# Optimization experiments

Measured on AMD Instinct MI355X. Metric: run time of the kernel, lower is better.

The kernel has to match this reference:

```python
import jax, jax.numpy as jnp
import numpy as np
import math

DEPTH = 3
NUM_GRAPHS = 8
BN_EPS = 1e-5
POOL_RATIO = 0.5


def _gcn(A, x, W, b):
    # GCNConv(improved=True): A_hat = A + 2*I; out = D^-1/2 A_hat D^-1/2 (x W) + b
    n = A.shape[0]
    A_hat = A + 2.0 * jnp.eye(n, dtype=A.dtype)
    deg = A_hat.sum(axis=1)
    d = jnp.where(deg > 0, jax.lax.rsqrt(deg), 0.0)
    return d[:, None] * (A_hat @ (d[:, None] * (x @ W))) + b


def _bn_eval(x, g, b):
    # BatchNorm1d in eval mode with running_mean=0, running_var=1
    return x * (g / jnp.sqrt(1.0 + BN_EPS)) + b


def _forward(x, edge_index, batch, conv0_w, conv0_b, down_w, down_b, pool_w,
             up_w, up_b, lins_w, lins_b, bn_g, bn_b, out_w, out_b):
    n0 = x.shape[0]
    # dense weighted adjacency A[dst, src] += 1 (duplicates sum, same as scatter-add MP)
    A = jnp.zeros((n0, n0), x.dtype).at[edge_index[1], edge_index[0]].add(1.0)

    # ---- GraphUNet (eval mode: dropout p=0.92 is identity) ----
    h = jax.nn.relu(_gcn(A, x, conv0_w, conv0_b))
    xs, As, perms = [h], [A], []
    for i in range(DEPTH):
        n = A.shape[0]
        eye = jnp.eye(n, dtype=A.dtype)
        S = A + eye                       # add_self_loops(weight=1)
        A2 = (S @ S) * (1.0 - eye)        # spspmm then remove_self_loops
        # TopKPooling: score = tanh((x.w)/||w||), keep top ceil(0.5*n) nodes
        score = jnp.tanh((h @ pool_w[i]) / jnp.linalg.norm(pool_w[i]))
        k = math.ceil(POOL_RATIO * n)
        _, perm = jax.lax.top_k(score, k)
        h = h[perm] * score[perm][:, None]
        A = A2[perm][:, perm]             # filter_adj
        h = jax.nn.relu(_gcn(A, h, down_w[i], down_b[i]))
        if i < DEPTH - 1:
            xs.append(h)
            As.append(A)
        perms.append(perm)
    for i in range(DEPTH):
        j = DEPTH - 1 - i
        res, Aj, perm = xs[j], As[j], perms[j]
        up = jnp.zeros_like(res).at[perm].set(h)
        h = res + up                      # sum_res=True skip connection
        h = _gcn(Aj, h, up_w[i], up_b[i])
        if i < DEPTH - 1:
            h = jax.nn.relu(h)

    # ---- global_add_pool + BN/Linear/tanh head ----
    g = jax.ops.segment_sum(h, batch, num_segments=NUM_GRAPHS)
    for i in range(3):
        g = _bn_eval(g, bn_g[i], bn_b[i])
        g = jnp.tanh(g @ lins_w[i] + lins_b[i])
    g = _bn_eval(g, bn_g[3], bn_b[3])
    return g @ out_w + out_b


def setup_inputs() -> dict:
    key = jax.random.key(0)
    ks = jax.random.split(key, 20)
    N, F, H, O, E = 4096, 64, 128, 32, 65536
    s = 0.05
    x = jax.random.normal(ks[0], (N, F), jnp.float32)
    src = jax.random.randint(ks[1], (E,), 0, N)
    dst = jax.random.randint(ks[2], (E,), 0, N)
    edge_index = jnp.stack([jnp.concatenate([src, dst]),
                            jnp.concatenate([dst, src])]).astype(jnp.int32)
    batch = jnp.sort(jax.random.randint(ks[3], (N,), 0, NUM_GRAPHS)).astype(jnp.int32)
    return {
        "x": x,
        "edge_index": edge_index,
        "batch": batch,
        "conv0_w": jax.random.normal(ks[4], (F, H), jnp.float32) * s,
        "conv0_b": jnp.zeros((H,), jnp.float32),
        "down_w": jax.random.normal(ks[5], (DEPTH, H, H), jnp.float32) * s,
        "down_b": jnp.zeros((DEPTH, H), jnp.float32),
        "pool_w": jax.random.normal(ks[6], (DEPTH, H), jnp.float32),
        "up_w": jax.random.normal(ks[7], (DEPTH, H, H), jnp.float32) * s,
        "up_b": jnp.zeros((DEPTH, H), jnp.float32),
        "lins_w": jax.random.normal(ks[8], (3, H, H), jnp.float32) * s,
        "lins_b": jnp.zeros((3, H), jnp.float32),
        "bn_g": jnp.ones((4, H), jnp.float32),
        "bn_b": jnp.zeros((4, H), jnp.float32),
        "out_w": jax.random.normal(ks[9], (H, O), jnp.float32) * s,
        "out_b": jnp.zeros((O,), jnp.float32),
    }


def reference(x, edge_index, batch, conv0_w, conv0_b, down_w, down_b, pool_w,
              up_w, up_b, lins_w, lins_b, bn_g, bn_b, out_w, out_b):
    return _forward(x, edge_index, batch, conv0_w, conv0_b, down_w, down_b,
                    pool_w, up_w, up_b, lins_w, lins_b, bn_g, bn_b, out_w, out_b)
```

## Files before the change

kernel.cpp:

```cpp
#include <hip/hip_runtime.h>
#include <math.h>

#define H 128
#define NG 8

typedef __attribute__((ext_vector_type(8))) short bf16x8;
typedef __attribute__((ext_vector_type(8))) unsigned short ushort8;
typedef __attribute__((ext_vector_type(4))) float f32x4;

static __device__ __forceinline__ float b2f(unsigned short u) {
  union { unsigned int i; float f; } v;
  v.i = ((unsigned int)u) << 16;
  return v.f;
}
static __device__ __forceinline__ unsigned short f2b(float f) {
  return (unsigned short)(__float_as_uint(f) >> 16);
}

__global__ void k_hist(const int* __restrict__ ei, int E, int* __restrict__ cnt) {
  int e = blockIdx.x * 256 + threadIdx.x;
  if (e >= E) return;
  atomicAdd(&cnt[ei[E + e]], 1);
}

__global__ __launch_bounds__(1024) void k_scan(const int* __restrict__ cnt,
                                               int* __restrict__ rowptr,
                                               float* __restrict__ dv, int n) {
  __shared__ int sums[1024];
  int tid = threadIdx.x;
  int base = tid * 4;
  int v0 = 0, v1 = 0, v2 = 0, v3 = 0;
  if (base < n) { v0 = cnt[base]; v1 = cnt[base + 1]; v2 = cnt[base + 2]; v3 = cnt[base + 3]; }
  int s = v0 + v1 + v2 + v3;
  sums[tid] = s;
  __syncthreads();
  for (int off = 1; off < 1024; off <<= 1) {
    int t = (tid >= off) ? sums[tid - off] : 0;
    __syncthreads();
    sums[tid] += t;
    __syncthreads();
  }
  int excl = sums[tid] - s;
  if (base < n) {
    rowptr[base] = excl;
    rowptr[base + 1] = excl + v0;
    rowptr[base + 2] = excl + v0 + v1;
    rowptr[base + 3] = excl + v0 + v1 + v2;
    dv[base] = rsqrtf((float)v0 + 2.0f);
    dv[base + 1] = rsqrtf((float)v1 + 2.0f);
    dv[base + 2] = rsqrtf((float)v2 + 2.0f);
    dv[base + 3] = rsqrtf((float)v3 + 2.0f);
  }
  if (tid == 1023) rowptr[n] = sums[1023];
}

__global__ void k_fill(const int* __restrict__ ei, int E, const int* __restrict__ rowptr,
                       int* __restrict__ cursor, int* __restrict__ colidx) {
  int e = blockIdx.x * 256 + threadIdx.x;
  if (e >= E) return;
  int r = ei[E + e], c = ei[e];
  int p = atomicAdd(&cursor[r], 1);
  colidx[rowptr[r] + p] = c;
}

template <int MODE, int RS, int EMIT>
__global__ __launch_bounds__(256) void k_xw(const float* __restrict__ X,
                                            const float* __restrict__ W,
                                            const float* __restrict__ dv,
                                            const int* __restrict__ idx,
                                            const float* __restrict__ aux,
                                            float* __restrict__ Y,
                                            unsigned short* __restrict__ YT,
                                            int n, int F) {
  __shared__ float Xs[64][36];
  __shared__ float Ws[32][132];
  __shared__ int ridx[64];
  __shared__ float rscl[64];
  int tid = threadIdx.x;
  int rowBase = blockIdx.x * 64;
  if (MODE == 1) {
    if (tid < 64) {
      int pp = idx[rowBase + tid];
      ridx[tid] = pp;
      rscl[tid] = aux[pp];
    }
  } else if (MODE == 2) {
    if (tid < 64) ridx[tid] = idx[rowBase + tid];
  }
  if (MODE != 0) __syncthreads();
  int r0 = (tid >> 5) << 3;
  int c0 = (tid & 31) << 2;
  float acc[8][4] = {};
  for (int k0 = 0; k0 < F; k0 += 32) {
#pragma unroll
    for (int it = 0, e = tid; it < 8; ++it, e += 256) {
      int ii = e >> 5, kk = e & 31;
      int gk = k0 + kk;
      float v;
      if (MODE == 0) {
        v = X[(size_t)(rowBase + ii) * F + gk];
      } else if (MODE == 1) {
        v = X[(size_t)ridx[ii] * F + gk] * rscl[ii];
      } else {
        v = X[(size_t)(rowBase + ii) * F + gk];
        int iv = ridx[ii];
        if (iv >= 0) v += aux[(size_t)iv * H + gk];
      }
      Xs[ii][kk] = v;
    }
#pragma unroll
    for (int it = 0, e = tid; it < 4; ++it, e += 256) {
      int kk = e >> 5, cc4 = e & 31;
      *(float4*)&Ws[kk][cc4 << 2] = *(const float4*)&W[(size_t)(k0 + kk) * H + (cc4 << 2)];
    }
    __syncthreads();
#pragma unroll
    for (int kk = 0; kk < 32; kk += 4) {
      float4 a4[8], w4[4];
#pragma unroll
      for (int i = 0; i < 8; ++i) a4[i] = *(const float4*)&Xs[r0 + i][kk];
#pragma unroll
      for (int s = 0; s < 4; ++s) w4[s] = *(const float4*)&Ws[kk + s][c0];
#pragma unroll
      for (int i = 0; i < 8; ++i) {
        float av[4] = {a4[i].x, a4[i].y, a4[i].z, a4[i].w};
#pragma unroll
        for (int s = 0; s < 4; ++s) {
          float wv[4] = {w4[s].x, w4[s].y, w4[s].z, w4[s].w};
#pragma unroll
          for (int j = 0; j < 4; ++j) acc[i][j] = fmaf(av[s], wv[j], acc[i][j]);
        }
      }
    }
    __syncthreads();
  }
  float vout[8][4];
#pragma unroll
  for (int i = 0; i < 8; ++i) {
    int row = rowBase + r0 + i;
    float d = RS ? rsqrtf(dv[row] + 2.0f) : dv[row];
#pragma unroll
    for (int j = 0; j < 4; ++j) vout[i][j] = d * acc[i][j];
    *(float4*)&Y[(size_t)row * H + c0] =
        make_float4(vout[i][0], vout[i][1], vout[i][2], vout[i][3]);
  }
  if (EMIT) {
#pragma unroll
    for (int j = 0; j < 4; ++j) {
      ushort8 hi, lo;
#pragma unroll
      for (int i = 0; i < 8; ++i) {
        float v = vout[i][j];
        unsigned short hh = f2b(v);
        hi[i] = hh;
        lo[i] = f2b(v - b2f(hh));
      }
      int c = c0 + j;
      *(ushort8*)&YT[(size_t)c * (2 * n) + rowBase + r0] = hi;
      *(ushort8*)&YT[(size_t)c * (2 * n) + n + rowBase + r0] = lo;
    }
  }
}

template <int SCORE>
__global__ void k_spmm_fin(const int* __restrict__ rowptr, const int* __restrict__ colidx,
                           const float* __restrict__ Y, const float* __restrict__ dv,
                           const float* __restrict__ bias, float* __restrict__ Out,
                           const float* __restrict__ w, float* __restrict__ score,
                           int n, int relu) {
  __shared__ float wn;
  int tid = threadIdx.x;
  if (SCORE) {
    if (tid < 64) {
      float s = w[tid] * w[tid] + w[tid + 64] * w[tid + 64];
#pragma unroll
      for (int o = 32; o > 0; o >>= 1) s += __shfl_down(s, o);
      if (tid == 0) wn = sqrtf(s);
    }
    __syncthreads();
  }
  int row = blockIdx.x * 4 + (tid >> 6);
  int lane = tid & 63;
  if (row >= n) return;
  int s = rowptr[row], e = rowptr[row + 1];
  int c2 = lane * 2;
  float a0 = 0.f, a1 = 0.f;
  int i = s;
  for (; i + 1 < e; i += 2) {
    int cA = colidx[i], cB = colidx[i + 1];
    float2 yA = *(const float2*)&Y[(size_t)cA * H + c2];
    float2 yB = *(const float2*)&Y[(size_t)cB * H + c2];
    a0 += yA.x + yB.x;
    a1 += yA.y + yB.y;
  }
  if (i < e) {
    int c = colidx[i];
    float2 y = *(const float2*)&Y[(size_t)c * H + c2];
    a0 += y.x;
    a1 += y.y;
  }
  float d = dv[row];
  float2 yr = *(const float2*)&Y[(size_t)row * H + c2];
  float v0 = d * (a0 + 2.0f * yr.x) + bias[c2];
  float v1 = d * (a1 + 2.0f * yr.y) + bias[c2 + 1];
  if (relu) { v0 = fmaxf(v0, 0.f); v1 = fmaxf(v1, 0.f); }
  *(float2*)&Out[(size_t)row * H + c2] = make_float2(v0, v1);
  if (SCORE) {
    float sc = v0 * w[c2] + v1 * w[c2 + 1];
#pragma unroll
    for (int o = 32; o > 0; o >>= 1) sc += __shfl_down(sc, o);
    if (lane == 0) score[row] = tanhf(sc / wn);
  }
}

__global__ __launch_bounds__(256) void k_ata_rows(const int* __restrict__ rowptr,
                                                  const int* __restrict__ colidx,
                                                  const int* __restrict__ perm,
                                                  const int* __restrict__ inv,
                                                  unsigned short* __restrict__ Ab,
                                                  float* __restrict__ dv, int kdim) {
  __shared__ int acc[2048];
  __shared__ int wsum[4];
  int i = blockIdx.x;
  int tid = threadIdx.x;
  for (int j = tid; j < kdim; j += 256) acc[j] = 0;
  __syncthreads();
  int p = perm[i];
  int s = rowptr[p], e = rowptr[p + 1];
  int deg = e - s;
  int wave = tid >> 6, lane = tid & 63;
  for (int q = wave; q <= deg; q += 4) {
    int kn = (q < deg) ? colidx[s + q] : p;
    int s2 = rowptr[kn], e2 = rowptr[kn + 1];
    for (int idx = s2 + lane; idx <= e2; idx += 64) {
      int j = (idx < e2) ? colidx[idx] : kn;
      int ii = inv[j];
      if (ii >= 0) atomicAdd(&acc[ii], 1);
    }
  }
  __syncthreads();
  int rs = 0;
  {
    int j0 = tid * 8;
    ushort8 v;
#pragma unroll
    for (int q = 0; q < 8; ++q) {
      int j = j0 + q;
      int c = (j == i) ? 0 : acc[j];
      rs += c;
      v[q] = f2b((float)c);
    }
    *(ushort8*)&Ab[(size_t)i * kdim + j0] = v;
  }
#pragma unroll
  for (int o = 32; o > 0; o >>= 1) rs += __shfl_down(rs, o);
  if (lane == 0) wsum[wave] = rs;
  __syncthreads();
  if (tid == 0) dv[i] = rsqrtf((float)(wsum[0] + wsum[1] + wsum[2] + wsum[3]) + 2.0f);
}

__global__ __launch_bounds__(256) void k_ata_mfma_g(const unsigned short* __restrict__ Ab,
                                                    const int* __restrict__ perm,
                                                    float* __restrict__ PartC,
                                                    int n, int k, int KC) {
  __shared__ __align__(16) unsigned short As[64][64];
  __shared__ __align__(16) unsigned short Bs[64][64];
  __shared__ int pr[64], pc[64];
  int tid = threadIdx.x;
  int w = tid >> 6, ln = tid & 63;
  int l15 = ln & 15, l4 = ln >> 4;
  int br = blockIdx.y, bc = blockIdx.x;
  if (tid < 64) pr[tid] = perm[br * 64 + tid];
  else if (tid < 128) pc[tid - 64] = perm[bc * 64 + (tid - 64)];
  __syncthreads();
  f32x4 acc[4] = {};
  int k0s = blockIdx.z * KC;
  for (int k0 = k0s; k0 < k0s + KC; k0 += 64) {
#pragma unroll
    for (int it = 0; it < 2; ++it) {
      int e = tid + it * 256;
      int row = e >> 3, ch = e & 7;
      int sch = (ch ^ (row & 7)) * 8;
      int base = k0 + ch * 8;
      {
        int p = pr[row];
        ushort8 v = *(const ushort8*)&Ab[(size_t)p * n + base];
#pragma unroll
        for (int q = 0; q < 8; ++q)
          if (base + q == p) v[q] = f2b(b2f(v[q]) + 1.0f);
        *(ushort8*)&As[row][sch] = v;
      }
      {
        int p = pc[row];
        ushort8 v = *(const ushort8*)&Ab[(size_t)p * n + base];
#pragma unroll
        for (int q = 0; q < 8; ++q)
          if (base + q == p) v[q] = f2b(b2f(v[q]) + 1.0f);
        *(ushort8*)&Bs[row][sch] = v;
      }
    }
    __syncthreads();
#pragma unroll
    for (int s = 0; s < 2; ++s) {
      int arow = w * 16 + l15;
      bf16x8 af = *(const bf16x8*)&As[arow][((s * 4 + l4) ^ (arow & 7)) * 8];
#pragma unroll
      for (int f = 0; f < 4; ++f) {
        int brow = f * 16 + l15;
        bf16x8 bfr = *(const bf16x8*)&Bs[brow][((s * 4 + l4) ^ (brow & 7)) * 8];
        acc[f] = __builtin_amdgcn_mfma_f32_16x16x32_bf16(af, bfr, acc[f], 0, 0, 0);
      }
    }
    __syncthreads();
  }
  float* out = PartC + (size_t)blockIdx.z * k * k;
#pragma unroll
  for (int f = 0; f < 4; ++f) {
#pragma unroll
    for (int r = 0; r < 4; ++r) {
      int gi = br * 64 + w * 16 + l4 * 4 + r;
      int gj = bc * 64 + f * 16 + l15;
      out[(size_t)gi * k + gj] = acc[f][r];
    }
  }
}

__global__ __launch_bounds__(256) void k_ata_sk_part(const float* __restrict__ A,
                                                     const int* __restrict__ perm,
                                                     float* __restrict__ PartC,
                                                     int n, int k, int CK) {
  int bc = blockIdx.x, br = blockIdx.y;
  __shared__ float As[64][36];
  __shared__ float Bs[64][36];
  __shared__ int pr[64], pc[64];
  int tid = threadIdx.x;
  if (tid < 64) pr[tid] = perm[br * 64 + tid];
  else if (tid < 128) pc[tid - 64] = perm[bc * 64 + (tid - 64)];
  __syncthreads();
  int ty = tid >> 4;
  int tx = tid & 15;
  float acc[4][4] = {};
  int k0s = blockIdx.z * CK;
  for (int k0 = k0s; k0 < k0s + CK; k0 += 32) {
#pragma unroll
    for (int it = 0, e = tid; it < 8; ++it, e += 256) {
      int ii = e >> 5, kk = e & 31;
      int gk = k0 + kk;
      int p = pr[ii];
      As[ii][kk] = A[(size_t)p * n + gk] + ((p == gk) ? 1.0f : 0.0f);
      p = pc[ii];
      Bs[ii][kk] = A[(size_t)p * n + gk] + ((p == gk) ? 1.0f : 0.0f);
    }
    __syncthreads();
#pragma unroll
    for (int kk = 0; kk < 32; kk += 4) {
      float4 a4[4], b4[4];
#pragma unroll
      for (int i = 0; i < 4; ++i) a4[i] = *(const float4*)&As[ty + 16 * i][kk];
#pragma unroll
      for (int j = 0; j < 4; ++j) b4[j] = *(const float4*)&Bs[tx + 16 * j][kk];
#pragma unroll
      for (int i = 0; i < 4; ++i) {
        float av[4] = {a4[i].x, a4[i].y, a4[i].z, a4[i].w};
#pragma unroll
        for (int j = 0; j < 4; ++j) {
          float bv[4] = {b4[j].x, b4[j].y, b4[j].z, b4[j].w};
#pragma unroll
          for (int s = 0; s < 4; ++s) acc[i][j] = fmaf(av[s], bv[s], acc[i][j]);
        }
      }
    }
    __syncthreads();
  }
  float* out = PartC + (size_t)blockIdx.z * k * k;
#pragma unroll
  for (int i = 0; i < 4; ++i) {
    int gi = br * 64 + ty + 16 * i;
#pragma unroll
    for (int j = 0; j < 4; ++j) {
      int gj = bc * 64 + tx + 16 * j;
      out[(size_t)gi * k + gj] = acc[i][j];
    }
  }
}

template <int NCH>
__global__ void k_ata_fin(const float* __restrict__ PartC, float* __restrict__ C,
                          float* __restrict__ rowsum, int k) {
  __shared__ float wsum[4];
  int gi = blockIdx.x;
  int tid = threadIdx.x;
  int j4 = tid * 4;
  size_t stride = (size_t)k * k;
  size_t off = (size_t)gi * k + j4;
  float4 s = *(const float4*)&PartC[off];
#pragma unroll
  for (int z = 1; z < NCH; ++z) {
    float4 p = *(const float4*)&PartC[z * stride + off];
    s.x += p.x; s.y += p.y; s.z += p.z; s.w += p.w;
  }
  if (gi >= j4 && gi < j4 + 4) ((float*)&s)[gi - j4] = 0.0f;
  *(float4*)&C[off] = s;
  float part = s.x + s.y + s.z + s.w;
  int lane = tid & 63, wave = tid >> 6;
#pragma unroll
  for (int o = 32; o > 0; o >>= 1) part += __shfl_down(part, o);
  if (lane == 0) wsum[wave] = part;
  __syncthreads();
  if (tid == 0) {
    int nw = blockDim.x >> 6;
    float t = 0.f;
    for (int q = 0; q < nw; ++q) t += wsum[q];
    rowsum[gi] = t;
  }
}

__global__ __launch_bounds__(256) void k_gcn_mfma(const unsigned short* __restrict__ A,
                                                  const unsigned short* __restrict__ YT,
                                                  float* __restrict__ Part, int n, int VK) {
  __shared__ __align__(16) unsigned short As[64][64];
  __shared__ __align__(16) unsigned short Bs[128][64];
  int tid = threadIdx.x;
  int w = tid >> 6, ln = tid & 63;
  int l15 = ln & 15, l4 = ln >> 4;
  int rowBase = blockIdx.x * 64;
  float* out = Part + (size_t)blockIdx.y * n * H;
  f32x4 acc[8] = {};
  int vk0s = blockIdx.y * VK;
  for (int vk0 = vk0s; vk0 < vk0s + VK; vk0 += 64) {
    int ka = vk0 & (n - 1);
#pragma unroll
    for (int it = 0; it < 2; ++it) {
      int e = tid + it * 256;
      int row = e >> 3, ch = e & 7;
      int sch = (ch ^ (row & 7)) * 8;
      *(ushort8*)&As[row][sch] = *(const ushort8*)&A[(size_t)(rowBase + row) * n + ka + ch * 8];
    }
#pragma unroll
    for (int it = 0; it < 4; ++it) {
      int e = tid + it * 256;
      int row = e >> 3, ch = e & 7;
      int sch = (ch ^ (row & 7)) * 8;
      *(ushort8*)&Bs[row][sch] = *(const ushort8*)&YT[(size_t)row * (2 * n) + vk0 + ch * 8];
    }
    __syncthreads();
#pragma unroll
    for (int s = 0; s < 2; ++s) {
      int arow = w * 16 + l15;
      bf16x8 af = *(const bf16x8*)&As[arow][((s * 4 + l4) ^ (arow & 7)) * 8];
#pragma unroll
      for (int f = 0; f < 8; ++f) {
        int brow = f * 16 + l15;
        bf16x8 bfr = *(const bf16x8*)&Bs[brow][((s * 4 + l4) ^ (brow & 7)) * 8];
        acc[f] = __builtin_amdgcn_mfma_f32_16x16x32_bf16(af, bfr, acc[f], 0, 0, 0);
      }
    }
    __syncthreads();
  }
#pragma unroll
  for (int f = 0; f < 8; ++f) {
#pragma unroll
    for (int r = 0; r < 4; ++r) {
      int row = rowBase + w * 16 + l4 * 4 + r;
      out[(size_t)row * H + f * 16 + l15] = acc[f][r];
    }
  }
}

__global__ __launch_bounds__(256) void k_gcn_part(const float* __restrict__ A,
                                                  const float* __restrict__ Y,
                                                  float* __restrict__ Part,
                                                  int n, int KC) {
  __shared__ float As[64][36];
  __shared__ float Ys[32][132];
  int tid = threadIdx.x;
  int r0 = (tid >> 5) << 3;
  int c0 = (tid & 31) << 2;
  size_t rowBase = (size_t)blockIdx.x * 64;
  int k0s = blockIdx.y * KC;
  float* out = Part + (size_t)blockIdx.y * n * H;
  float acc[8][4] = {};
  for (int k0 = k0s; k0 < k0s + KC; k0 += 32) {
#pragma unroll
    for (int it = 0, e = tid; it < 8; ++it, e += 256) {
      int ii = e >> 5, kk = e & 31;
      As[ii][kk] = A[(rowBase + ii) * (size_t)n + k0 + kk];
    }
#pragma unroll
    for (int it = 0, e = tid; it < 4; ++it, e += 256) {
      int kk = e >> 5, cc4 = e & 31;
      *(float4*)&Ys[kk][cc4 << 2] = *(const float4*)&Y[(size_t)(k0 + kk) * H + (cc4 << 2)];
    }
    __syncthreads();
#pragma unroll
    for (int kk = 0; kk < 32; kk += 4) {
      float4 a4[8], y4[4];
#pragma unroll
      for (int i = 0; i < 8; ++i) a4[i] = *(const float4*)&As[r0 + i][kk];
#pragma unroll
      for (int s = 0; s < 4; ++s) y4[s] = *(const float4*)&Ys[kk + s][c0];
#pragma unroll
      for (int i = 0; i < 8; ++i) {
        float av[4] = {a4[i].x, a4[i].y, a4[i].z, a4[i].w};
#pragma unroll
        for (int s = 0; s < 4; ++s) {
          float yv[4] = {y4[s].x, y4[s].y, y4[s].z, y4[s].w};
#pragma unroll
          for (int j = 0; j < 4; ++j) acc[i][j] = fmaf(av[s], yv[j], acc[i][j]);
        }
      }
    }
    __syncthreads();
  }
#pragma unroll
  for (int i = 0; i < 8; ++i) {
    size_t row = rowBase + r0 + i;
    *(float4*)&out[row * H + c0] = make_float4(acc[i][0], acc[i][1], acc[i][2], acc[i][3]);
  }
}

template <int RS, int SCORE>
__global__ void k_gcn_fin(const float* __restrict__ Part, const float* __restrict__ Y,
                          const float* __restrict__ dv, const float* __restrict__ bias,
                          float* __restrict__ Out,
                          const float* __restrict__ w, float* __restrict__ score,
                          int n, int nch, int relu) {
  __shared__ float wn;
  int tid = threadIdx.x;
  if (SCORE) {
    if (tid < 64) {
      float s = w[tid] * w[tid] + w[tid + 64] * w[tid + 64];
#pragma unroll
      for (int o = 32; o > 0; o >>= 1) s += __shfl_down(s, o);
      if (tid == 0) wn = sqrtf(s);
    }
    __syncthreads();
  }
  int i4 = blockIdx.x * 256 + tid;
  int row = i4 >> 5, c4 = (i4 & 31) * 4;
  size_t stride = (size_t)n * H;
  float4 s = *(const float4*)&Part[i4 * 4];
  for (int c = 1; c < nch; ++c) {
    float4 p = *(const float4*)&Part[c * stride + i4 * 4];
    s.x += p.x; s.y += p.y; s.z += p.z; s.w += p.w;
  }
  float4 y = *(const float4*)&Y[i4 * 4];
  float d = RS ? rsqrtf(dv[row] + 2.0f) : dv[row];
  float4 v;
  v.x = d * (s.x + 2.0f * y.x) + bias[c4];
  v.y = d * (s.y + 2.0f * y.y) + bias[c4 + 1];
  v.z = d * (s.z + 2.0f * y.z) + bias[c4 + 2];
  v.w = d * (s.w + 2.0f * y.w) + bias[c4 + 3];
  if (relu) {
    v.x = fmaxf(v.x, 0.f); v.y = fmaxf(v.y, 0.f);
    v.z = fmaxf(v.z, 0.f); v.w = fmaxf(v.w, 0.f);
  }
  *(float4*)&Out[i4 * 4] = v;
  if (SCORE) {
    float sc = v.x * w[c4] + v.y * w[c4 + 1] + v.z * w[c4 + 2] + v.w * w[c4 + 3];
#pragma unroll
    for (int o = 16; o > 0; o >>= 1) sc += __shfl_down(sc, o, 32);
    if ((tid & 31) == 0) score[row] = tanhf(sc / wn);
  }
}

static __device__ __forceinline__ void ce_(unsigned long long& x, unsigned long long& y, bool asc) {
  if ((x < y) != asc) { unsigned long long t = x; x = y; y = t; }
}
static __device__ __forceinline__ unsigned long long pick_(unsigned long long a,
                                                           unsigned long long b,
                                                           bool lower, bool asc) {
  unsigned long long lo = (a < b) ? a : b;
  unsigned long long hi = (a < b) ? b : a;
  return (lower == asc) ? lo : hi;
}

template <int LOGN>
__global__ __launch_bounds__(1024) void k_topk(const float* __restrict__ score,
                                               int* __restrict__ perm,
                                               int* __restrict__ inv) {
  const int n = 1 << LOGN;
  __shared__ unsigned long long lds[1 << LOGN];
  int t = threadIdx.x;
  int e0 = t * 4;
  unsigned long long key[4];
#pragma unroll
  for (int j = 0; j < 4; ++j) {
    unsigned u = __float_as_uint(score[e0 + j]);
    u = (u & 0x80000000u) ? ~u : (u | 0x80000000u);
    u = ~u;
    key[j] = (((unsigned long long)u) << 32) | (unsigned)(e0 + j);
  }
  ce_(key[0], key[1], true);
  ce_(key[2], key[3], false);
  for (int size = 4; size <= n; size <<= 1) {
    bool asc = ((e0 & size) == 0);
    for (int stride = size >> 1; stride >= 256; stride >>= 1) {
#pragma unroll
      for (int j = 0; j < 4; ++j) lds[e0 + j] = key[j];
      __syncthreads();
      bool lower = ((e0 & stride) == 0);
#pragma unroll
      for (int j = 0; j < 4; ++j)
        key[j] = pick_(key[j], lds[(e0 + j) ^ stride], lower, asc);
      __syncthreads();
    }
    int s0 = ((size >> 1) < 256) ? (size >> 1) : 128;
    for (int stride = s0; stride >= 4; stride >>= 1) {
      int m = stride >> 2;
      bool lower = ((t & m) == 0);
#pragma unroll
      for (int j = 0; j < 4; ++j) {
        unsigned long long o = __shfl_xor(key[j], m, 64);
        key[j] = pick_(key[j], o, lower, asc);
      }
    }
    ce_(key[0], key[2], asc);
    ce_(key[1], key[3], asc);
    ce_(key[0], key[1], asc);
    ce_(key[2], key[3], asc);
  }
  int kk = n >> 1;
#pragma unroll
  for (int j = 0; j < 4; ++j) {
    int e = e0 + j;
    int idx = (int)(key[j] & 0xffffffffu);
    if (e < kk) perm[e] = idx;
    if (inv) inv[idx] = (e < kk) ? e : -1;
  }
}

__global__ void k_segsum(const float* __restrict__ h, const int* __restrict__ batch,
                         float* __restrict__ g, int n) {
  int c = threadIdx.x;
  int r0 = blockIdx.x * 32;
  int rend = min(r0 + 32, n);
  float acc = 0.f;
  int cur = batch[r0];
  for (int r = r0; r < rend; ++r) {
    int b = batch[r];
    if (b != cur) { atomicAdd(&g[cur * H + c], acc); acc = 0.f; cur = b; }
    acc += h[(size_t)r * H + c];
  }
  atomicAdd(&g[cur * H + c], acc);
}

__global__ __launch_bounds__(256) void k_head(const float* __restrict__ g,
    const float* __restrict__ lins_w, const float* __restrict__ lins_b,
    const float* __restrict__ bn_g, const float* __restrict__ bn_b,
    const float* __restrict__ out_w, const float* __restrict__ out_b,
    float* __restrict__ out) {
  __shared__ float a[NG * H], b[NG * H];
  int tid = threadIdx.x;
  const float inv = 1.0f / sqrtf(1.0f + 1e-5f);
  for (int i = tid; i < NG * H; i += 256) a[i] = g[i];
  __syncthreads();
  for (int L = 0; L < 3; ++L) {
    for (int i = tid; i < NG * H; i += 256) {
      int c = i & 127;
      b[i] = a[i] * (bn_g[L * H + c] * inv) + bn_b[L * H + c];
    }
    __syncthreads();
    for (int i = tid; i < NG * H; i += 256) {
      int r = i >> 7, c = i & 127;
      float s = lins_b[L * H + c];
      for (int k2 = 0; k2 < H; ++k2) s += b[r * H + k2] * lins_w[(size_t)L * H * H + k2 * H + c];
      a[i] = tanhf(s);
    }
    __syncthreads();
  }
  for (int i = tid; i < NG * H; i += 256) {
    int c = i & 127;
    b[i] = a[i] * (bn_g[3 * H + c] * inv) + bn_b[3 * H + c];
  }
  __syncthreads();
  for (int i = tid; i < NG * 32; i += 256) {
    int r = i >> 5, o = i & 31;
    float s = out_b[o];
    for (int k2 = 0; k2 < H; ++k2) s += b[r * H + k2] * out_w[k2 * 32 + o];
    out[i] = s;
  }
}

extern "C" void kernel_launch(void* const* d_in, const int* in_sizes, int n_in,
                              void* d_out, int out_size, void* d_ws, size_t ws_size,
                              hipStream_t stream) {
  const float* x       = (const float*)d_in[0];
  const int*   ei      = (const int*)d_in[1];
  const int*   batch   = (const int*)d_in[2];
  const float* conv0_w = (const float*)d_in[3];
  const float* conv0_b = (const float*)d_in[4];
  const float* down_w  = (const float*)d_in[5];
  const float* down_b  = (const float*)d_in[6];
  const float* pool_w  = (const float*)d_in[7];
  const float* up_w    = (const float*)d_in[8];
  const float* up_b    = (const float*)d_in[9];
  const float* lins_w  = (const float*)d_in[10];
  const float* lins_b  = (const float*)d_in[11];
  const float* bn_g    = (const float*)d_in[12];
  const float* bn_b    = (const float*)d_in[13];
  const float* out_w   = (const float*)d_in[14];
  const float* out_b   = (const float*)d_in[15];
  int E = in_sizes[1] / 2;

  char* p = (char*)d_ws;
  auto alloc = [&](size_t bytes) {
    char* r = p;
    p += (bytes + 255) & ~(size_t)255;
    return r;
  };
  unsigned short* A1b  = (unsigned short*)alloc((size_t)2048 * 2048 * 2);
  unsigned short* YT   = (unsigned short*)alloc((size_t)128 * 4096 * 2);
  float*          A2m  = (float*)alloc((size_t)1024 * 1024 * 4);
  float*          A3   = (float*)alloc((size_t)512 * 512 * 4);
  float*          part = (float*)alloc((size_t)16 * 1024 * 1024 * 4);
  int* cnt    = (int*)alloc(4096 * 4);
  int* cursor = (int*)alloc(4096 * 4);
  int* rowptr = (int*)alloc(4100 * 4);
  int* colidx = (int*)alloc((size_t)E * 4);
  int* inv0   = (int*)alloc(4096 * 4);
  int* inv1   = (int*)alloc(2048 * 4);
  int* inv2   = (int*)alloc(1024 * 4);
  float* dv0  = (float*)alloc(4096 * 4);
  float* dv1  = (float*)alloc(2048 * 4);
  float* dv2  = (float*)alloc(1024 * 4);
  float* dv3  = (float*)alloc(512 * 4);
  int* perm0  = (int*)alloc(2048 * 4);
  int* perm1  = (int*)alloc(1024 * 4);
  int* perm2  = (int*)alloc(512 * 4);
  float* score = (float*)alloc(4096 * 4);
  float* h0 = (float*)alloc((size_t)4096 * H * 4);
  float* h1 = (float*)alloc((size_t)2048 * H * 4);
  float* h2 = (float*)alloc((size_t)1024 * H * 4);
  float* h3 = (float*)alloc((size_t)512 * H * 4);
  float* t2 = (float*)alloc((size_t)4096 * H * 4);
  float* hu = (float*)alloc((size_t)4096 * H * 4);
  float* g  = (float*)alloc(NG * H * 4);

  hipMemsetAsync(cnt, 0, 2 * 4096 * 4, stream);
  k_hist<<<(E + 255) / 256, 256, 0, stream>>>(ei, E, cnt);
  k_scan<<<1, 1024, 0, stream>>>(cnt, rowptr, dv0, 4096);
  k_fill<<<(E + 255) / 256, 256, 0, stream>>>(ei, E, rowptr, cursor, colidx);

  k_xw<0, 0, 0><<<4096 / 64, 256, 0, stream>>>(x, conv0_w, dv0, nullptr, nullptr, t2, nullptr, 4096, 64);
  k_spmm_fin<1><<<1024, 256, 0, stream>>>(rowptr, colidx, t2, dv0, conv0_b, h0, pool_w, score, 4096, 1);

  k_topk<12><<<1, 1024, 0, stream>>>(score, perm0, inv0);
  k_ata_rows<<<2048, 256, 0, stream>>>(rowptr, colidx, perm0, inv0, A1b, dv1, 2048);
  k_xw<1, 0, 1><<<2048 / 64, 256, 0, stream>>>(h0, down_w, dv1, perm0, score, t2, YT, 2048, 128);
  k_gcn_mfma<<<dim3(2048 / 64, 16), 256, 0, stream>>>(A1b, YT, part, 2048, 4096 / 16);
  k_gcn_fin<0, 1><<<2048 / 8, 256, 0, stream>>>(part, t2, dv1, down_b, h1, pool_w + H, score, 2048, 16, 1);

  k_topk<11><<<1, 512, 0, stream>>>(score, perm1, inv1);
  k_ata_mfma_g<<<dim3(16, 16, 4), 256, 0, stream>>>(A1b, perm1, part, 2048, 1024, 512);
  k_ata_fin<4><<<1024, 256, 0, stream>>>(part, A2m, dv2, 1024);
  k_xw<1, 1, 0><<<1024 / 64, 256, 0, stream>>>(h1, down_w + (size_t)H * H, dv2, perm1, score, t2, nullptr, 1024, 128);
  k_gcn_part<<<dim3(1024 / 64, 8), 256, 0, stream>>>(A2m, t2, part, 1024, 128);
  k_gcn_fin<1, 1><<<1024 / 8, 256, 0, stream>>>(part, t2, dv2, down_b + H, h2, pool_w + 2 * H, score, 1024, 8, 1);

  k_topk<10><<<1, 256, 0, stream>>>(score, perm2, inv2);
  k_ata_sk_part<<<dim3(8, 8, 8), 256, 0, stream>>>(A2m, perm2, part, 1024, 512, 128);
  k_ata_fin<8><<<512, 128, 0, stream>>>(part, A3, dv3, 512);
  k_xw<1, 1, 0><<<512 / 64, 256, 0, stream>>>(h2, down_w + (size_t)2 * H * H, dv3, perm2, score, t2, nullptr, 512, 128);
  k_gcn_part<<<dim3(512 / 64, 8), 256, 0, stream>>>(A3, t2, part, 512, 64);
  k_gcn_fin<1, 0><<<512 / 8, 256, 0, stream>>>(part, t2, dv3, down_b + 2 * H, h3, nullptr, nullptr, 512, 8, 1);

  k_xw<2, 1, 0><<<1024 / 64, 256, 0, stream>>>(h2, up_w, dv2, inv2, h3, t2, nullptr, 1024, 128);
  k_gcn_part<<<dim3(1024 / 64, 8), 256, 0, stream>>>(A2m, t2, part, 1024, 128);
  k_gcn_fin<1, 0><<<1024 / 8, 256, 0, stream>>>(part, t2, dv2, up_b, hu, nullptr, nullptr, 1024, 8, 1);

  k_xw<2, 0, 1><<<2048 / 64, 256, 0, stream>>>(h1, up_w + (size_t)H * H, dv1, inv1, hu, t2, YT, 2048, 128);
  k_gcn_mfma<<<dim3(2048 / 64, 16), 256, 0, stream>>>(A1b, YT, part, 2048, 4096 / 16);
  k_gcn_fin<0, 0><<<2048 / 8, 256, 0, stream>>>(part, t2, dv1, up_b + H, hu, nullptr, nullptr, 2048, 16, 1);

  k_xw<2, 0, 0><<<4096 / 64, 256, 0, stream>>>(h0, up_w + (size_t)2 * H * H, dv0, inv0, hu, t2, nullptr, 4096, 128);
  k_spmm_fin<0><<<1024, 256, 0, stream>>>(rowptr, colidx, t2, dv0, up_b + 2 * H, hu, nullptr, nullptr, 4096, 0);

  hipMemsetAsync(g, 0, NG * H * 4, stream);
  k_segsum<<<4096 / 32, 128, 0, stream>>>(hu, batch, g, 4096);
  k_head<<<1, 256, 0, stream>>>(g, lins_w, lins_b, bn_g, bn_b, out_w, out_b, (float*)d_out);
}
```

Before: 522.9 us.

## Replace single-block bitonic top-k with multi-block rank counting

Replaces the single-workgroup bitonic sort used for top-k pooling with a rank-by-counting kernel spread over n/256 blocks. Each block loads all keys into shared memory and each thread counts how many keys are smaller than its own, which gives its rank directly. This removes the serial sort stages and barriers on one CU in exchange for O(n^2) comparisons spread across more blocks. Every block redundantly loads all n keys.

```diff
diff --git a/kernel.cpp b/kernel.cpp
--- a/kernel.cpp
+++ b/kernel.cpp
@@ -564,70 +564,29 @@
   }
 }
 
-static __device__ __forceinline__ void ce_(unsigned long long& x, unsigned long long& y, bool asc) {
-  if ((x < y) != asc) { unsigned long long t = x; x = y; y = t; }
-}
-static __device__ __forceinline__ unsigned long long pick_(unsigned long long a,
-                                                           unsigned long long b,
-                                                           bool lower, bool asc) {
-  unsigned long long lo = (a < b) ? a : b;
-  unsigned long long hi = (a < b) ? b : a;
-  return (lower == asc) ? lo : hi;
-}
-
-template <int LOGN>
-__global__ __launch_bounds__(1024) void k_topk(const float* __restrict__ score,
-                                               int* __restrict__ perm,
-                                               int* __restrict__ inv) {
-  const int n = 1 << LOGN;
-  __shared__ unsigned long long lds[1 << LOGN];
-  int t = threadIdx.x;
-  int e0 = t * 4;
-  unsigned long long key[4];
-#pragma unroll
-  for (int j = 0; j < 4; ++j) {
-    unsigned u = __float_as_uint(score[e0 + j]);
+__global__ __launch_bounds__(256) void k_topk_rank(const float* __restrict__ score,
+                                                   int* __restrict__ perm,
+                                                   int* __restrict__ inv, int n) {
+  __shared__ unsigned long long keys[4096];
+  int tid = threadIdx.x;
+  for (int i = tid; i < n; i += 256) {
+    unsigned u = __float_as_uint(score[i]);
     u = (u & 0x80000000u) ? ~u : (u | 0x80000000u);
     u = ~u;
-    key[j] = (((unsigned long long)u) << 32) | (unsigned)(e0 + j);
-  }
-  ce_(key[0], key[1], true);
-  ce_(key[2], key[3], false);
-  for (int size = 4; size <= n; size <<= 1) {
-    bool asc = ((e0 & size) == 0);
-    for (int stride = size >> 1; stride >= 256; stride >>= 1) {
-#pragma unroll
-      for (int j = 0; j < 4; ++j) lds[e0 + j] = key[j];
-      __syncthreads();
-      bool lower = ((e0 & stride) == 0);
-#pragma unroll
-      for (int j = 0; j < 4; ++j)
-        key[j] = pick_(key[j], lds[(e0 + j) ^ stride], lower, asc);
-      __syncthreads();
-    }
-    int s0 = ((size >> 1) < 256) ? (size >> 1) : 128;
-    for (int stride = s0; stride >= 4; stride >>= 1) {
-      int m = stride >> 2;
-      bool lower = ((t & m) == 0);
-#pragma unroll
-      for (int j = 0; j < 4; ++j) {
-        unsigned long long o = __shfl_xor(key[j], m, 64);
-        key[j] = pick_(key[j], o, lower, asc);
-      }
-    }
-    ce_(key[0], key[2], asc);
-    ce_(key[1], key[3], asc);
-    ce_(key[0], key[1], asc);
-    ce_(key[2], key[3], asc);
+    keys[i] = (((unsigned long long)u) << 32) | (unsigned)i;
+  }
+  __syncthreads();
+  int gid = blockIdx.x * 256 + tid;
+  unsigned long long my = keys[gid];
+  int rank = 0;
+  for (int j = 0; j < n; j += 8) {
+#pragma unroll
+    for (int q = 0; q < 8; ++q) rank += (keys[j + q] < my) ? 1 : 0;
   }
   int kk = n >> 1;
-#pragma unroll
-  for (int j = 0; j < 4; ++j) {
-    int e = e0 + j;
-    int idx = (int)(key[j] & 0xffffffffu);
-    if (e < kk) perm[e] = idx;
-    if (inv) inv[idx] = (e < kk) ? e : -1;
-  }
+  int idx = (int)(my & 0xffffffffu);
+  if (rank < kk) perm[rank] = idx;
+  inv[idx] = (rank < kk) ? rank : -1;
 }
 
 __global__ void k_segsum(const float* __restrict__ h, const int* __restrict__ batch,
@@ -745,20 +704,20 @@
   k_xw<0, 0, 0><<<4096 / 64, 256, 0, stream>>>(x, conv0_w, dv0, nullptr, nullptr, t2, nullptr, 4096, 64);
   k_spmm_fin<1><<<1024, 256, 0, stream>>>(rowptr, colidx, t2, dv0, conv0_b, h0, pool_w, score, 4096, 1);
 
-  k_topk<12><<<1, 1024, 0, stream>>>(score, perm0, inv0);
+  k_topk_rank<<<4096 / 256, 256, 0, stream>>>(score, perm0, inv0, 4096);
   k_ata_rows<<<2048, 256, 0, stream>>>(rowptr, colidx, perm0, inv0, A1b, dv1, 2048);
   k_xw<1, 0, 1><<<2048 / 64, 256, 0, stream>>>(h0, down_w, dv1, perm0, score, t2, YT, 2048, 128);
   k_gcn_mfma<<<dim3(2048 / 64, 16), 256, 0, stream>>>(A1b, YT, part, 2048, 4096 / 16);
   k_gcn_fin<0, 1><<<2048 / 8, 256, 0, stream>>>(part, t2, dv1, down_b, h1, pool_w + H, score, 2048, 16, 1);
 
-  k_topk<11><<<1, 512, 0, stream>>>(score, perm1, inv1);
+  k_topk_rank<<<2048 / 256, 256, 0, stream>>>(score, perm1, inv1, 2048);
   k_ata_mfma_g<<<dim3(16, 16, 4), 256, 0, stream>>>(A1b, perm1, part, 2048, 1024, 512);
   k_ata_fin<4><<<1024, 256, 0, stream>>>(part, A2m, dv2, 1024);
   k_xw<1, 1, 0><<<1024 / 64, 256, 0, stream>>>(h1, down_w + (size_t)H * H, dv2, perm1, score, t2, nullptr, 1024, 128);
   k_gcn_part<<<dim3(1024 / 64, 8), 256, 0, stream>>>(A2m, t2, part, 1024, 128);
   k_gcn_fin<1, 1><<<1024 / 8, 256, 0, stream>>>(part, t2, dv2, down_b + H, h2, pool_w + 2 * H, score, 1024, 8, 1);
 
-  k_topk<10><<<1, 256, 0, stream>>>(score, perm2, inv2);
+  k_topk_rank<<<1024 / 256, 256, 0, stream>>>(score, perm2, inv2, 1024);
   k_ata_sk_part<<<dim3(8, 8, 8), 256, 0, stream>>>(A2m, perm2, part, 1024, 512, 128);
   k_ata_fin<8><<<512, 128, 0, stream>>>(part, A3, dv3, 512);
   k_xw<1, 1, 0><<<512 / 64, 256, 0, stream>>>(h2, down_w + (size_t)2 * H * H, dv3, perm2, score, t2, nullptr, 512, 128);
```

Measured after the change: 525.7 us. About the same (+0.5%).
